# Kernel tuning notes

Measured on AMD Instinct MI355X. Metric: run time of the kernel, lower is better.

## Reference

```python
import jax, jax.numpy as jnp
import numpy as np

XYZ_MIN = -1.0
XYZ_MAX = 1.0
MULTIRES = 4  # viewdirs positional-embedding frequencies


def trilerp(grid, pts):
    """Trilinear interpolation, align_corners=True, border clamp.
    grid: [C, X, Y, Z]; pts: [N, 3] in world coords. Returns [N, C]."""
    res = np.array(grid.shape[1:])  # (X, Y, Z)
    resf = jnp.asarray(res, dtype=pts.dtype)
    u = (pts - XYZ_MIN) / (XYZ_MAX - XYZ_MIN) * (resf - 1.0)  # [N,3] voxel coords
    u = jnp.clip(u, 0.0, resf - 1.0)
    i0 = jnp.clip(jnp.floor(u).astype(jnp.int32), 0, jnp.asarray(res - 2, dtype=jnp.int32))
    f = u - i0.astype(pts.dtype)  # [N,3] fractional offsets
    out = 0.0
    for dx in (0, 1):
        wx = f[:, 0] if dx else 1.0 - f[:, 0]
        for dy in (0, 1):
            wy = f[:, 1] if dy else 1.0 - f[:, 1]
            for dz in (0, 1):
                wz = f[:, 2] if dz else 1.0 - f[:, 2]
                g = grid[:, i0[:, 0] + dx, i0[:, 1] + dy, i0[:, 2] + dz]  # [C,N]
                out = out + (wx * wy * wz) * g
    return out.T  # [N,C]


def embed_viewdirs(v):
    """NeRF positional embedding: [v, sin(2^k v), cos(2^k v)] -> [N, 3+3*2*MULTIRES]."""
    freqs = 2.0 ** jnp.arange(MULTIRES, dtype=v.dtype)  # [F]
    ang = v[:, None, :] * freqs[None, :, None]  # [N,F,3]
    n = v.shape[0]
    return jnp.concatenate([v, jnp.sin(ang).reshape(n, -1), jnp.cos(ang).reshape(n, -1)], axis=-1)


def setup_inputs() -> dict:
    key = jax.random.key(0)
    ks = jax.random.split(key, 8)
    n = 2097152
    pts = jax.random.uniform(ks[0], (n, 3), jnp.float32, minval=XYZ_MIN, maxval=XYZ_MAX)
    vd = jax.random.normal(ks[1], (n, 3), jnp.float32)
    viewdirs = vd / jnp.linalg.norm(vd, axis=-1, keepdims=True)
    density_grid = jax.random.normal(ks[2], (1, 160, 160, 160), jnp.float32)
    color_grid = jax.random.normal(ks[3], (12, 160, 160, 160), jnp.float32)
    in_dim = 9 + 3 + 3 * 2 * MULTIRES  # k0_view (12-3) + viewdirs embed (27) = 36
    w0 = jax.random.normal(ks[4], (in_dim, 128), jnp.float32) * (1.0 / np.sqrt(in_dim))
    w1 = jax.random.normal(ks[5], (128, 128), jnp.float32) * (1.0 / np.sqrt(128))
    w2 = jax.random.normal(ks[6], (128, 3), jnp.float32) * (1.0 / np.sqrt(128))
    return {
        "pts": pts, "viewdirs": viewdirs,
        "density_grid": density_grid, "color_grid": color_grid,
        "w0": w0, "b0": jnp.zeros((128,), jnp.float32),
        "w1": w1, "b1": jnp.zeros((128,), jnp.float32),
        "w2": w2, "b2": jnp.zeros((3,), jnp.float32),
    }


def reference(pts, viewdirs, density_grid, color_grid, w0, b0, w1, b1, w2, b2):
    # density branch (use_densitynet=False -> raw interpolated density, channels=1)
    pts_density = trilerp(density_grid, pts)  # [N,1]
    # color branch with color_emission: k0 = [diffuse(3), view-dep(9)]
    k0 = trilerp(color_grid, pts)  # [N,12]
    k0_diffuse, k0_view = k0[:, :3], k0[:, 3:]
    feat = jnp.concatenate([k0_view, embed_viewdirs(viewdirs)], axis=-1)  # [N,36]
    h = jax.nn.relu(feat @ w0 + b0)
    h = jax.nn.relu(h @ w1 + b1)
    k0_logit = h @ w2 + b2  # [N,3]
    pts_color = jax.nn.sigmoid(k0_logit + k0_diffuse)
    return jnp.concatenate([pts_color, pts_density], axis=-1)  # [N,4]
```

## Files before the change

### kernel.cpp

```cpp
#include <hip/hip_runtime.h>
#include <hip/hip_bf16.h>
#include <math.h>

#define RES   160
#define RES2  (160*160)
#define RES3  (160*160*160)
#define TG_ELEMS ((size_t)RES3 * 16)
#define TG_BYTES (TG_ELEMS * 2)

#define CG16_BYTES ((size_t)RES3 * 16)

#define BLOB_BYTES  47104
#define BLOB_SHORTS 22528
#define BLOB_FLOATS 512
#define A1_OFF      12288
#define B1P_OFF     45056
#define W2P_OFF     45568

typedef __attribute__((ext_vector_type(8)))  short s16x8;
typedef __attribute__((ext_vector_type(2)))  float f32x2;
typedef __attribute__((ext_vector_type(4)))  float f32x4;
typedef __attribute__((ext_vector_type(16))) float f32x16;
typedef __attribute__((ext_vector_type(4)))  int   i32x4;

__device__ __forceinline__ unsigned short f2bf(float x) {
    union { float f; unsigned u; } v; v.f = x;
    unsigned r = v.u + 0x7FFFu + ((v.u >> 16) & 1u);
    return (unsigned short)(r >> 16);
}
__device__ __forceinline__ unsigned cvtpk(float lo, float hi) {
    unsigned r;
    asm("v_cvt_pk_bf16_f32 %0, %1, %2" : "=v"(r) : "v"(lo), "v"(hi));
    return r;
}
__device__ __forceinline__ float bf_lo(unsigned u) {
    union { unsigned u; float f; } v; v.u = u << 16; return v.f;
}
__device__ __forceinline__ float bf_hi(unsigned u) {
    union { unsigned u; float f; } v; v.u = u & 0xFFFF0000u; return v.f;
}
__device__ __forceinline__ unsigned cvtpk_relu(float a, float b) {
    return cvtpk(fmaxf(a, 0.0f), fmaxf(b, 0.0f));
}
__device__ __forceinline__ void plswap(unsigned &a, unsigned &b) {
    asm("v_permlane32_swap_b32 %0, %1" : "+v"(a), "+v"(b));
}
__device__ __forceinline__ float sum_halves(float x) {
    unsigned a = __float_as_uint(x), b = a;
    plswap(a, b);
    return __uint_as_float(a) + __uint_as_float(b);
}
__device__ __forceinline__ f32x2 pkfma(f32x2 a, f32x2 b, f32x2 c) {
    f32x2 r;
    asm("v_pk_fma_f32 %0, %1, %2, %3" : "=v"(r) : "v"(a), "v"(b), "v"(c));
    return r;
}
__device__ __forceinline__ f32x2 pkmul(f32x2 a, f32x2 b) {
    f32x2 r;
    asm("v_pk_mul_f32 %0, %1, %2" : "=v"(r) : "v"(a), "v"(b));
    return r;
}

__device__ __forceinline__ unsigned enc8_manual(float x) {
    unsigned u = __float_as_uint(x);
    unsigned s = (u >> 24) & 0x80u;
    unsigned mag = u & 0x7FFFFFFFu;
    if (mag < 0x3C800000u) return s;
    if (mag >= 0x43E00000u) return s | 0x7Eu;
    unsigned r = mag + 0x7FFFFu + ((mag >> 20) & 1u);
    return s | ((r >> 20) - 960u);
}
__device__ __forceinline__ float dec8_manual(unsigned b) {
    unsigned s = (b & 0x80u) << 24;
    unsigned em = b & 0x7Fu;
    if (em == 0) return __uint_as_float(s);
    if (em < 8) {
        float v = (float)em * 0.001953125f;
        return (b & 0x80u) ? -v : v;
    }
    return __uint_as_float(s | ((em + 960u) << 20));
}
template<bool HI>
__device__ __forceinline__ unsigned pk_enc8(float a, float b, unsigned old) {
#if __has_builtin(__builtin_amdgcn_cvt_pk_fp8_f32)
    return (unsigned)__builtin_amdgcn_cvt_pk_fp8_f32(a, b, (int)old, HI);
#else
    unsigned w = enc8_manual(a) | (enc8_manual(b) << 8);
    return HI ? ((old & 0xFFFFu) | (w << 16)) : ((old & 0xFFFF0000u) | w);
#endif
}
template<bool HI>
__device__ __forceinline__ f32x2 pk_dec8(unsigned w) {
#if __has_builtin(__builtin_amdgcn_cvt_pk_f32_fp8)
    return __builtin_amdgcn_cvt_pk_f32_fp8((int)w, HI);
#else
    unsigned h = HI ? (w >> 16) : (w & 0xFFFFu);
    return f32x2{ dec8_manual(h & 0xFFu), dec8_manual((h >> 8) & 0xFFu) };
#endif
}

__device__ __forceinline__ float blob_short_val(int i, const float* __restrict__ w0,
                                                const float* __restrict__ b0,
                                                const float* __restrict__ w1) {
    if (i < 6144) {
        int e = i & 7, s = i >> 3;
        int lo = s & 31, r = s >> 5;
        int hi = r & 1, t = r >> 1;
        int wm = t / 3, ks = t - wm * 3;
        int k = ks * 16 + hi * 8 + e, n = wm * 32 + lo;
        return k < 36 ? w0[k * 128 + n] : (k == 36 ? b0[n] : 0.0f);
    } else {
        int i2 = i - 6144;
        int e = i2 & 7, s = i2 >> 3;
        int lo = s & 31, r = s >> 5;
        int hi = r & 1, t = r >> 1;
        int wm = t >> 3, ks = t & 7;
        int k = ks * 16 + hi * 8 + e, n = wm * 32 + lo;
        return w1[k * 128 + n];
    }
}
__device__ __forceinline__ float blob_float_val(int j, const float* __restrict__ b1,
                                                const float* __restrict__ w2) {
    if (j < 128) {
        int c = j & 3, r = j >> 2, hi = r & 1, t = r >> 1;
        int g = t & 3, wm = t >> 2;
        return b1[wm * 32 + 8 * g + 4 * hi + c];
    } else {
        int j2 = j - 128;
        int c  = j2 & 3;
        int t  = j2 >> 2;
        int cc = t % 3;
        int u  = t / 3;
        int hi = u & 1, v = u >> 1;
        int g  = v & 3, wm = v >> 2;
        return w2[(wm * 32 + 8 * g + 4 * hi + c) * 3 + cc];
    }
}

__global__ __launch_bounds__(256) void make_tg(
    const float* __restrict__ dgrid, const float* __restrict__ cgrid,
    short* __restrict__ tg)
{
    const int v = blockIdx.x * 256 + threadIdx.x;
    float vals[13];
    #pragma unroll
    for (int c = 0; c < 12; ++c) vals[c] = cgrid[(size_t)c * RES3 + v];
    vals[12] = dgrid[v];

    i32x4 r0 = { (int)cvtpk(vals[0], vals[1]),  (int)cvtpk(vals[2],  vals[3]),
                 (int)cvtpk(vals[4], vals[5]),  (int)cvtpk(vals[6],  vals[7]) };
    i32x4 r1 = { (int)cvtpk(vals[8], vals[9]),  (int)cvtpk(vals[10], vals[11]),
                 (int)cvtpk(vals[12], 0.0f),    0 };
    *(i32x4*)&tg[(size_t)v * 16 + 0] = r0;
    *(i32x4*)&tg[(size_t)v * 16 + 8] = r1;
}

__global__ __launch_bounds__(256) void make_cg16(
    const float* __restrict__ dgrid, const float* __restrict__ cgrid,
    char* __restrict__ cg16)
{
    const int v = blockIdx.x * 256 + threadIdx.x;
    float vals[13];
    #pragma unroll
    for (int c = 0; c < 12; ++c) vals[c] = cgrid[(size_t)c * RES3 + v];
    vals[12] = dgrid[v];

    unsigned w0 = pk_enc8<false>(vals[3], vals[4], 0u);
    w0 = pk_enc8<true>(vals[5], vals[6], w0);
    unsigned w1 = pk_enc8<false>(vals[7], vals[8], 0u);
    w1 = pk_enc8<true>(vals[9], vals[10], w1);
    unsigned w2 = pk_enc8<false>(vals[11], vals[0], 0u);
    w2 = pk_enc8<true>(vals[1], vals[2], w2);
    unsigned w3 = (unsigned)f2bf(vals[12]);

    i32x4 r = { (int)w0, (int)w1, (int)w2, (int)w3 };
    *(i32x4*)(cg16 + (size_t)v * 16) = r;
}

__global__ __launch_bounds__(256) void prepack(
    const float* __restrict__ w0, const float* __restrict__ b0,
    const float* __restrict__ w1, const float* __restrict__ b1,
    const float* __restrict__ w2, char* __restrict__ blob)
{
    int t = blockIdx.x * 256 + threadIdx.x;
    if (t < BLOB_SHORTS) {
        ((short*)blob)[t] = (short)f2bf(blob_short_val(t, w0, b0, w1));
    } else if (t < BLOB_SHORTS + BLOB_FLOATS) {
        int j = t - BLOB_SHORTS;
        ((float*)(blob + B1P_OFF))[j] = blob_float_val(j, b1, w2);
    }
}

template<int MODE, bool PRE>
__global__ __launch_bounds__(512, 4) void dvgo_fused(
    const float* __restrict__ pts, const float* __restrict__ vdirs,
    const float* __restrict__ dgrid, const float* __restrict__ cgrid,
    const short* __restrict__ tg, const char* __restrict__ cg16,
    const char* __restrict__ blob,
    const float* __restrict__ w0, const float* __restrict__ b0,
    const float* __restrict__ w1, const float* __restrict__ b1,
    const float* __restrict__ w2, const float* __restrict__ b2,
    float* __restrict__ out)
{
    __shared__ __align__(16) char smem[BLOB_BYTES];
    const int tid  = threadIdx.x;
    const int lane = tid & 63;
    const int wv   = tid >> 6;
    const int lo   = lane & 31;
    const int hi   = lane >> 5;

    if (PRE) {
        const i32x4* src = (const i32x4*)blob;
        i32x4* dst = (i32x4*)smem;
        for (int i = tid; i < BLOB_BYTES / 16; i += 512) dst[i] = src[i];
    } else {
        for (int i = tid; i < BLOB_SHORTS; i += 512)
            ((short*)smem)[i] = (short)f2bf(blob_short_val(i, w0, b0, w1));
        for (int i = tid; i < BLOB_FLOATS; i += 512)
            ((float*)(smem + B1P_OFF))[i] = blob_float_val(i, b1, w2);
    }

    const int p = blockIdx.x * 512 + tid;
    float P0 = pts[p*3+0], P1 = pts[p*3+1], P2 = pts[p*3+2];
    float V0 = vdirs[p*3+0], V1 = vdirs[p*3+1], V2 = vdirs[p*3+2];

    int   ii[3];
    float ff[3];
    float Pv[3] = {P0, P1, P2};
    #pragma unroll
    for (int d = 0; d < 3; ++d) {
        float u = (Pv[d] + 1.0f) * 79.5f;
        u = fminf(fmaxf(u, 0.0f), 159.0f);
        int i0 = (int)u;
        if (i0 > 158) i0 = 158;
        ii[d] = i0;
        ff[d] = u - (float)i0;
    }
    const float fx = ff[0], fy = ff[1], fz = ff[2];
    const float wxy0 = (1.0f-fx)*(1.0f-fy);
    const float wxy1 = (1.0f-fx)*fy;
    const float wxy2 = fx*(1.0f-fy);
    const float wxy3 = fx*fy;

    float dens;
    float col[12];

    if (MODE == 2) {
        const size_t vidx = (size_t)(ii[0] * RES + ii[1]) * RES + ii[2];
        const char* q00 = cg16 + vidx * 16;
        const char* q01 = q00 + (size_t)RES * 16;
        const char* q10 = q00 + (size_t)RES2 * 16;
        const char* q11 = q10 + (size_t)RES * 16;

        f32x2 cv[7];
        #pragma unroll
        for (int pr = 0; pr < 7; ++pr) cv[pr] = f32x2{0.0f, 0.0f};
        float densacc = 0.0f;

        const char* qs[4] = { q00, q01, q10, q11 };
        const float wsx[4] = { wxy0, wxy1, wxy2, wxy3 };
        #pragma unroll
        for (int cn = 0; cn < 4; ++cn) {
            const char* q = qs[cn];
            i32x4 A = *(const i32x4*)(q);
            i32x4 B = *(const i32x4*)(q + 16);
            const f32x2 wv2 = { wsx[cn], wsx[cn] };

            f32x2 a, b, lz;
            a = pk_dec8<false>((unsigned)A[0]); b = pk_dec8<false>((unsigned)B[0]);
            lz = pkfma(f32x2{fz,fz}, f32x2{b.x-a.x, b.y-a.y}, a);
            cv[0] = pkfma(wv2, lz, cv[0]);
            a = pk_dec8<true >((unsigned)A[0]); b = pk_dec8<true >((unsigned)B[0]);
            lz = pkfma(f32x2{fz,fz}, f32x2{b.x-a.x, b.y-a.y}, a);
            cv[1] = pkfma(wv2, lz, cv[1]);
            a = pk_dec8<false>((unsigned)A[1]); b = pk_dec8<false>((unsigned)B[1]);
            lz = pkfma(f32x2{fz,fz}, f32x2{b.x-a.x, b.y-a.y}, a);
            cv[2] = pkfma(wv2, lz, cv[2]);
            a = pk_dec8<true >((unsigned)A[1]); b = pk_dec8<true >((unsigned)B[1]);
            lz = pkfma(f32x2{fz,fz}, f32x2{b.x-a.x, b.y-a.y}, a);
            cv[3] = pkfma(wv2, lz, cv[3]);
            a = pk_dec8<false>((unsigned)A[2]); b = pk_dec8<false>((unsigned)B[2]);
            lz = pkfma(f32x2{fz,fz}, f32x2{b.x-a.x, b.y-a.y}, a);
            cv[4] = pkfma(wv2, lz, cv[4]);
            a = pk_dec8<true >((unsigned)A[2]); b = pk_dec8<true >((unsigned)B[2]);
            lz = pkfma(f32x2{fz,fz}, f32x2{b.x-a.x, b.y-a.y}, a);
            cv[5] = pkfma(wv2, lz, cv[5]);
            float da = bf_lo((unsigned)A[3]), db = bf_lo((unsigned)B[3]);
            densacc = __builtin_fmaf(wsx[cn], __builtin_fmaf(fz, db - da, da), densacc);
        }
        col[3] = cv[0].x; col[4]  = cv[0].y;
        col[5] = cv[1].x; col[6]  = cv[1].y;
        col[7] = cv[2].x; col[8]  = cv[2].y;
        col[9] = cv[3].x; col[10] = cv[3].y;
        col[11] = cv[4].x; col[0] = cv[4].y;
        col[1] = cv[5].x; col[2]  = cv[5].y;
        dens = densacc;
    } else if (MODE == 1) {
        const int base16 = ((ii[0]*RES + ii[1])*RES + ii[2]) * 16;
        const short* q00 = tg + base16;
        const short* q01 = q00 + RES*16;
        const short* q10 = q00 + RES2*16;
        const short* q11 = q10 + RES*16;

        f32x2 cv[7];
        #pragma unroll
        for (int pr = 0; pr < 7; ++pr) cv[pr] = f32x2{0.0f, 0.0f};
        const f32x2 fzv   = { fz, fz };
        const f32x2 omfzv = { 1.0f - fz, 1.0f - fz };
        const short* qs[4] = { q00, q01, q10, q11 };
        const float  wsx[4] = { wxy0, wxy1, wxy2, wxy3 };
        #pragma unroll
        for (int cn = 0; cn < 4; ++cn) {
            const short* q = qs[cn];
            i32x4 u0 = *(const i32x4*)(q);
            i32x4 u1v = *(const i32x4*)(q + 8);
            i32x4 u2 = *(const i32x4*)(q + 16);
            i32x4 u3 = *(const i32x4*)(q + 24);
            unsigned av[8] = { (unsigned)u0[0], (unsigned)u0[1], (unsigned)u0[2], (unsigned)u0[3],
                               (unsigned)u1v[0], (unsigned)u1v[1], (unsigned)u1v[2], (unsigned)u1v[3] };
            unsigned bv[8] = { (unsigned)u2[0], (unsigned)u2[1], (unsigned)u2[2], (unsigned)u2[3],
                               (unsigned)u3[0], (unsigned)u3[1], (unsigned)u3[2], (unsigned)u3[3] };
            const f32x2 wv2 = { wsx[cn], wsx[cn] };
            #pragma unroll
            for (int pr = 0; pr < 7; ++pr) {
                f32x2 va = { bf_lo(av[pr]), bf_hi(av[pr]) };
                f32x2 vb = { bf_lo(bv[pr]), bf_hi(bv[pr]) };
                f32x2 lz = pkfma(fzv, vb, pkmul(omfzv, va));
                cv[pr] = pkfma(wv2, lz, cv[pr]);
            }
        }
        #pragma unroll
        for (int c = 0; c < 12; ++c) col[c] = (c & 1) ? cv[c >> 1].y : cv[c >> 1].x;
        dens = cv[6].x;
    } else {
        const int base = (ii[0]*RES + ii[1])*RES + ii[2];
        const int o0 = base, o1 = base + RES, o2 = base + RES2, o3 = base + RES2 + RES;
        auto tl = [&](const float* __restrict__ g) -> float {
            float a0 = g[o0], a1 = g[o0+1];
            float c0 = g[o1], c1 = g[o1+1];
            float d0 = g[o2], d1 = g[o2+1];
            float e0 = g[o3], e1 = g[o3+1];
            float v0 = a0 + fz*(a1-a0);
            float v1 = c0 + fz*(c1-c0);
            float v2 = d0 + fz*(d1-d0);
            float v3 = e0 + fz*(e1-e0);
            return wxy0*v0 + wxy1*v1 + wxy2*v2 + wxy3*v3;
        };
        dens = tl(dgrid);
        #pragma unroll
        for (int c = 0; c < 12; ++c) col[c] = tl(cgrid + (size_t)c * RES3);
    }

    float ft[36];
    #pragma unroll
    for (int j = 0; j < 9; ++j) ft[j] = col[3+j];
    ft[9] = V0; ft[10] = V1; ft[11] = V2;
    float Vv[3] = {V0, V1, V2};
    #pragma unroll
    for (int d = 0; d < 3; ++d) {
        float s1, c1;
        __sincosf(Vv[d], &s1, &c1);
        float s2 = 2.0f*s1*c1,  c2 = __builtin_fmaf(-2.0f*s1, s1, 1.0f);
        float s4 = 2.0f*s2*c2,  c4 = __builtin_fmaf(-2.0f*s2, s2, 1.0f);
        float s8 = 2.0f*s4*c4,  c8 = __builtin_fmaf(-2.0f*s4, s4, 1.0f);
        ft[12 + d] = s1; ft[15 + d] = s2; ft[18 + d] = s4; ft[21 + d] = s8;
        ft[24 + d] = c1; ft[27 + d] = c2; ft[30 + d] = c4; ft[33 + d] = c8;
    }
    unsigned fpk[24];
    #pragma unroll
    for (int j = 0; j < 18; ++j) fpk[j] = cvtpk(ft[2*j], ft[2*j+1]);
    fpk[18] = cvtpk(1.0f, 0.0f);
    #pragma unroll
    for (int j = 19; j < 24; ++j) fpk[j] = 0u;

    #pragma unroll
    for (int ks = 0; ks < 3; ++ks)
        #pragma unroll
        for (int d = 0; d < 4; ++d)
            plswap(fpk[ks*8 + d], fpk[ks*8 + 4 + d]);

    const float col0v = col[0], col1v = col[1], col2v = col[2];
    const float scol0 = __shfl_xor(col0v, 32, 64);
    const float scol1 = __shfl_xor(col1v, 32, 64);
    const float scol2 = __shfl_xor(col2v, 32, 64);
    const float sdens = __shfl_xor(dens,  32, 64);
    const float b2v0 = b2[0], b2v1 = b2[1], b2v2 = b2[2];

    __syncthreads();

    const char*  a0p  = smem + lane * 16;
    const char*  a1p  = smem + A1_OFF + lane * 16;
    const float* b1ph = (const float*)(smem + B1P_OFF) + hi * 4;
    const float* w2ph = (const float*)(smem + W2P_OFF) + hi * 12;

    #pragma unroll
    for (int pt = 0; pt < 2; ++pt) {
        f32x16 acc0[4];
        #pragma unroll
        for (int w = 0; w < 4; ++w)
            #pragma unroll
            for (int r = 0; r < 16; ++r) acc0[w][r] = 0.0f;

        #pragma unroll
        for (int ks = 0; ks < 3; ++ks) {
            i32x4 bi = { (int)fpk[ks*8 + 4*pt + 0], (int)fpk[ks*8 + 4*pt + 1],
                         (int)fpk[ks*8 + 4*pt + 2], (int)fpk[ks*8 + 4*pt + 3] };
            s16x8 B = __builtin_bit_cast(s16x8, bi);
            #pragma unroll
            for (int w = 0; w < 4; ++w) {
                s16x8 A = *(const s16x8*)(a0p + (w*3 + ks) * 1024);
                acc0[w] = __builtin_amdgcn_mfma_f32_32x32x16_bf16(A, B, acc0[w], 0, 0, 0);
            }
        }

        unsigned u1[4][8];
        #pragma unroll
        for (int w = 0; w < 4; ++w)
            #pragma unroll
            for (int g = 0; g < 4; ++g) {
                u1[w][2*g+0] = cvtpk_relu(acc0[w][4*g+0], acc0[w][4*g+1]);
                u1[w][2*g+1] = cvtpk_relu(acc0[w][4*g+2], acc0[w][4*g+3]);
            }

        f32x16 acc1[4];
        #pragma unroll
        for (int w = 0; w < 4; ++w)
            #pragma unroll
            for (int g = 0; g < 4; ++g) {
                f32x4 bv = *(const f32x4*)(b1ph + (w*4 + g) * 8);
                acc1[w][4*g+0] = bv[0]; acc1[w][4*g+1] = bv[1];
                acc1[w][4*g+2] = bv[2]; acc1[w][4*g+3] = bv[3];
            }
        #pragma unroll
        for (int ks = 0; ks < 8; ++ks) {
            const int w = ks >> 1, q = 4 * (ks & 1);
            plswap(u1[w][q+0], u1[w][q+2]);
            plswap(u1[w][q+1], u1[w][q+3]);
            i32x4 bi = { (int)u1[w][q+0], (int)u1[w][q+1],
                         (int)u1[w][q+2], (int)u1[w][q+3] };
            s16x8 B = __builtin_bit_cast(s16x8, bi);
            #pragma unroll
            for (int wm = 0; wm < 4; ++wm) {
                s16x8 A = *(const s16x8*)(a1p + (wm*8 + ks) * 1024);
                acc1[wm] = __builtin_amdgcn_mfma_f32_32x32x16_bf16(A, B, acc1[wm], 0, 0, 0);
            }
        }

        f32x2 pa0 = {0.0f, 0.0f}, pa1 = {0.0f, 0.0f}, pa2 = {0.0f, 0.0f};
        #pragma unroll
        for (int w = 0; w < 4; ++w)
            #pragma unroll
            for (int g = 0; g < 4; ++g) {
                const float* wrow = w2ph + (w*4 + g) * 24;
                f32x4 q0 = *(const f32x4*)(wrow + 0);
                f32x4 q1 = *(const f32x4*)(wrow + 4);
                f32x4 q2 = *(const f32x4*)(wrow + 8);
                f32x2 v01 = { fmaxf(acc1[w][4*g+0], 0.0f), fmaxf(acc1[w][4*g+1], 0.0f) };
                f32x2 v23 = { fmaxf(acc1[w][4*g+2], 0.0f), fmaxf(acc1[w][4*g+3], 0.0f) };
                pa0 = pkfma(v01, f32x2{q0[0], q0[1]}, pa0);
                pa0 = pkfma(v23, f32x2{q0[2], q0[3]}, pa0);
                pa1 = pkfma(v01, f32x2{q1[0], q1[1]}, pa1);
                pa1 = pkfma(v23, f32x2{q1[2], q1[3]}, pa1);
                pa2 = pkfma(v01, f32x2{q2[0], q2[1]}, pa2);
                pa2 = pkfma(v23, f32x2{q2[2], q2[3]}, pa2);
            }
        float p0 = sum_halves(pa0.x + pa0.y);
        float p1 = sum_halves(pa1.x + pa1.y);
        float p2 = sum_halves(pa2.x + pa2.y);

        const float d0 = pt ? scol0 : col0v;
        const float d1 = pt ? scol1 : col1v;
        const float d2 = pt ? scol2 : col2v;
        const float dn = pt ? sdens : dens;
        if (hi == 0) {
            float x0 = p0 + b2v0 + d0;
            float x1 = p1 + b2v1 + d1;
            float x2 = p2 + b2v2 + d2;
            f32x4 o = { 1.0f / (1.0f + __expf(-x0)),
                        1.0f / (1.0f + __expf(-x1)),
                        1.0f / (1.0f + __expf(-x2)),
                        dn };
            const int gp = blockIdx.x * 512 + wv * 64 + pt * 32 + lo;
            *(f32x4*)(out + (size_t)gp * 4) = o;
        }
    }
}

extern "C" void kernel_launch(void* const* d_in, const int* in_sizes, int n_in,
                              void* d_out, int out_size, void* d_ws, size_t ws_size,
                              hipStream_t stream) {
    const float* pts = (const float*)d_in[0];
    const float* vd  = (const float*)d_in[1];
    const float* dg  = (const float*)d_in[2];
    const float* cg  = (const float*)d_in[3];
    const float* w0  = (const float*)d_in[4];
    const float* b0  = (const float*)d_in[5];
    const float* w1  = (const float*)d_in[6];
    const float* b1  = (const float*)d_in[7];
    const float* w2  = (const float*)d_in[8];
    const float* b2  = (const float*)d_in[9];
    float* out = (float*)d_out;

    const int n = in_sizes[0] / 3;
    const int blocks = n / 512;

    if (ws_size >= CG16_BYTES + BLOB_BYTES) {
        char* cg16 = (char*)d_ws;
        char* blob = (char*)d_ws + CG16_BYTES;
        make_cg16<<<RES3/256, 256, 0, stream>>>(dg, cg, cg16);
        prepack<<<(BLOB_SHORTS + BLOB_FLOATS + 255)/256, 256, 0, stream>>>(
            w0, b0, w1, b1, w2, blob);
        dvgo_fused<2, true><<<blocks, 512, 0, stream>>>(
            pts, vd, dg, cg, nullptr, cg16, blob, w0, b0, w1, b1, w2, b2, out);
    } else if (ws_size >= TG_BYTES + BLOB_BYTES) {
        short* tg = (short*)d_ws;
        char* blob = (char*)d_ws + TG_BYTES;
        make_tg<<<RES3/256, 256, 0, stream>>>(dg, cg, tg);
        prepack<<<(BLOB_SHORTS + BLOB_FLOATS + 255)/256, 256, 0, stream>>>(
            w0, b0, w1, b1, w2, blob);
        dvgo_fused<1, true><<<blocks, 512, 0, stream>>>(
            pts, vd, dg, cg, tg, nullptr, blob, w0, b0, w1, b1, w2, b2, out);
    } else if (ws_size >= TG_BYTES) {
        short* tg = (short*)d_ws;
        make_tg<<<RES3/256, 256, 0, stream>>>(dg, cg, tg);
        dvgo_fused<1, false><<<blocks, 512, 0, stream>>>(
            pts, vd, dg, cg, tg, nullptr, nullptr, w0, b0, w1, b1, w2, b2, out);
    } else {
        dvgo_fused<0, false><<<blocks, 512, 0, stream>>>(
            pts, vd, dg, cg, nullptr, nullptr, nullptr, w0, b0, w1, b1, w2, b2, out);
    }
}
```

Before: 246.2 us.

## Pack 2x2 yz-neighborhood per voxel into 64-byte records for trilinear gathers

Adds a preprocessing kernel that, for each voxel, stores the four y/z neighbours of all 12 colour channels in fp8 and the density in bf16, giving one 64-byte record per voxel. The fused kernel then needs only two contiguous 64-byte reads (x and x+1) per sample instead of four scattered 32-byte pairs, and interpolates with nested lerps. The cost is a four times larger intermediate grid (about 262 MB) to build each call and more preprocessing traffic, and the new path runs only when the workspace is large enough.

```diff
diff --git a/kernel.cpp b/kernel.cpp
--- a/kernel.cpp
+++ b/kernel.cpp
@@ -9,6 +9,8 @@
 #define TG_BYTES (TG_ELEMS * 2)
 
 #define CG16_BYTES ((size_t)RES3 * 16)
+
+#define QG64_BYTES ((size_t)RES3 * 64)
 
 #define BLOB_BYTES  47104
 #define BLOB_SHORTS 22528
@@ -97,6 +99,14 @@
     unsigned h = HI ? (w >> 16) : (w & 0xFFFFu);
     return f32x2{ dec8_manual(h & 0xFFu), dec8_manual((h >> 8) & 0xFFu) };
 #endif
+}
+
+__device__ __forceinline__ float quad_lerp(unsigned w, float fy, float fz) {
+    f32x2 lo = pk_dec8<false>(w);
+    f32x2 hi = pk_dec8<true >(w);
+    float vy0 = __builtin_fmaf(fz, lo.y - lo.x, lo.x);
+    float vy1 = __builtin_fmaf(fz, hi.y - hi.x, hi.x);
+    return __builtin_fmaf(fy, vy1 - vy0, vy0);
 }
 
 __device__ __forceinline__ float blob_short_val(int i, const float* __restrict__ w0,
@@ -177,6 +187,47 @@
     *(i32x4*)(cg16 + (size_t)v * 16) = r;
 }
 
+__global__ __launch_bounds__(256) void make_quad(
+    const float* __restrict__ dgrid, const float* __restrict__ cgrid,
+    char* __restrict__ qg)
+{
+    const int v = blockIdx.x * 256 + threadIdx.x;
+    const int z = v % RES;
+    const int xy = v / RES;
+    const int y = xy % RES;
+    const int dz = (z < RES-1) ? 1 : 0;
+    const int dy = (y < RES-1) ? RES : 0;
+    const int o00 = v, o01 = v + dz, o10 = v + dy, o11 = v + dy + dz;
+
+    unsigned words[16];
+    #pragma unroll
+    for (int c = 0; c < 13; ++c) {
+        float c00, c01, c10, c11;
+        if (c < 9) {
+            const float* g = cgrid + (size_t)(3 + c) * RES3;
+            c00 = g[o00]; c01 = g[o01]; c10 = g[o10]; c11 = g[o11];
+        } else if (c < 12) {
+            const float* g = cgrid + (size_t)(c - 9) * RES3;
+            c00 = g[o00]; c01 = g[o01]; c10 = g[o10]; c11 = g[o11];
+        } else {
+            c00 = c01 = c10 = c11 = 0.0f;
+        }
+        unsigned w = pk_enc8<false>(c00, c01, 0u);
+        words[c] = pk_enc8<true>(c10, c11, w);
+    }
+    words[13] = cvtpk(dgrid[o00], dgrid[o01]);
+    words[14] = cvtpk(dgrid[o10], dgrid[o11]);
+    words[15] = 0u;
+
+    char* dst = qg + (size_t)v * 64;
+    #pragma unroll
+    for (int s = 0; s < 4; ++s) {
+        i32x4 r = { (int)words[4*s+0], (int)words[4*s+1],
+                    (int)words[4*s+2], (int)words[4*s+3] };
+        *(i32x4*)(dst + s * 16) = r;
+    }
+}
+
 __global__ __launch_bounds__(256) void prepack(
     const float* __restrict__ w0, const float* __restrict__ b0,
     const float* __restrict__ w1, const float* __restrict__ b1,
@@ -195,7 +246,7 @@
 __global__ __launch_bounds__(512, 4) void dvgo_fused(
     const float* __restrict__ pts, const float* __restrict__ vdirs,
     const float* __restrict__ dgrid, const float* __restrict__ cgrid,
-    const short* __restrict__ tg, const char* __restrict__ cg16,
+    const short* __restrict__ tg, const char* __restrict__ gq,
     const char* __restrict__ blob,
     const float* __restrict__ w0, const float* __restrict__ b0,
     const float* __restrict__ w1, const float* __restrict__ b1,
@@ -237,17 +288,46 @@
         ff[d] = u - (float)i0;
     }
     const float fx = ff[0], fy = ff[1], fz = ff[2];
-    const float wxy0 = (1.0f-fx)*(1.0f-fy);
-    const float wxy1 = (1.0f-fx)*fy;
-    const float wxy2 = fx*(1.0f-fy);
-    const float wxy3 = fx*fy;
 
     float dens;
     float col[12];
 
-    if (MODE == 2) {
+    if (MODE == 3) {
         const size_t vidx = (size_t)(ii[0] * RES + ii[1]) * RES + ii[2];
-        const char* q00 = cg16 + vidx * 16;
+        const char* qa = gq + vidx * 64;
+        const char* qb = qa + (size_t)RES2 * 64;
+        i32x4 A[4], B[4];
+        #pragma unroll
+        for (int s = 0; s < 4; ++s) A[s] = *(const i32x4*)(qa + s * 16);
+        #pragma unroll
+        for (int s = 0; s < 4; ++s) B[s] = *(const i32x4*)(qb + s * 16);
+
+        #pragma unroll
+        for (int c = 0; c < 12; ++c) {
+            float va = quad_lerp((unsigned)A[c >> 2][c & 3], fy, fz);
+            float vb = quad_lerp((unsigned)B[c >> 2][c & 3], fy, fz);
+            float val = __builtin_fmaf(fx, vb - va, va);
+            if (c < 9) col[3 + c] = val;
+            else       col[c - 9] = val;
+        }
+        {
+            unsigned a13 = (unsigned)A[3][1], a14 = (unsigned)A[3][2];
+            unsigned b13 = (unsigned)B[3][1], b14 = (unsigned)B[3][2];
+            float ay0 = __builtin_fmaf(fz, bf_hi(a13) - bf_lo(a13), bf_lo(a13));
+            float ay1 = __builtin_fmaf(fz, bf_hi(a14) - bf_lo(a14), bf_lo(a14));
+            float va  = __builtin_fmaf(fy, ay1 - ay0, ay0);
+            float by0 = __builtin_fmaf(fz, bf_hi(b13) - bf_lo(b13), bf_lo(b13));
+            float by1 = __builtin_fmaf(fz, bf_hi(b14) - bf_lo(b14), bf_lo(b14));
+            float vb  = __builtin_fmaf(fy, by1 - by0, by0);
+            dens = __builtin_fmaf(fx, vb - va, va);
+        }
+    } else if (MODE == 2) {
+        const float wxy0 = (1.0f-fx)*(1.0f-fy);
+        const float wxy1 = (1.0f-fx)*fy;
+        const float wxy2 = fx*(1.0f-fy);
+        const float wxy3 = fx*fy;
+        const size_t vidx = (size_t)(ii[0] * RES + ii[1]) * RES + ii[2];
+        const char* q00 = gq + vidx * 16;
         const char* q01 = q00 + (size_t)RES * 16;
         const char* q10 = q00 + (size_t)RES2 * 16;
         const char* q11 = q10 + (size_t)RES * 16;
@@ -265,7 +345,6 @@
             i32x4 A = *(const i32x4*)(q);
             i32x4 B = *(const i32x4*)(q + 16);
             const f32x2 wv2 = { wsx[cn], wsx[cn] };
-
             f32x2 a, b, lz;
             a = pk_dec8<false>((unsigned)A[0]); b = pk_dec8<false>((unsigned)B[0]);
             lz = pkfma(f32x2{fz,fz}, f32x2{b.x-a.x, b.y-a.y}, a);
@@ -296,6 +375,10 @@
         col[1] = cv[5].x; col[2]  = cv[5].y;
         dens = densacc;
     } else if (MODE == 1) {
+        const float wxy0 = (1.0f-fx)*(1.0f-fy);
+        const float wxy1 = (1.0f-fx)*fy;
+        const float wxy2 = fx*(1.0f-fy);
+        const float wxy3 = fx*fy;
         const int base16 = ((ii[0]*RES + ii[1])*RES + ii[2]) * 16;
         const short* q00 = tg + base16;
         const short* q01 = q00 + RES*16;
@@ -333,6 +416,10 @@
         for (int c = 0; c < 12; ++c) col[c] = (c & 1) ? cv[c >> 1].y : cv[c >> 1].x;
         dens = cv[6].x;
     } else {
+        const float wxy0 = (1.0f-fx)*(1.0f-fy);
+        const float wxy1 = (1.0f-fx)*fy;
+        const float wxy2 = fx*(1.0f-fy);
+        const float wxy3 = fx*fy;
         const int base = (ii[0]*RES + ii[1])*RES + ii[2];
         const int o0 = base, o1 = base + RES, o2 = base + RES2, o3 = base + RES2 + RES;
         auto tl = [&](const float* __restrict__ g) -> float {
@@ -504,7 +591,15 @@
     const int n = in_sizes[0] / 3;
     const int blocks = n / 512;
 
-    if (ws_size >= CG16_BYTES + BLOB_BYTES) {
+    if (ws_size >= QG64_BYTES + BLOB_BYTES) {
+        char* qg = (char*)d_ws;
+        char* blob = (char*)d_ws + QG64_BYTES;
+        make_quad<<<RES3/256, 256, 0, stream>>>(dg, cg, qg);
+        prepack<<<(BLOB_SHORTS + BLOB_FLOATS + 255)/256, 256, 0, stream>>>(
+            w0, b0, w1, b1, w2, blob);
+        dvgo_fused<3, true><<<blocks, 512, 0, stream>>>(
+            pts, vd, dg, cg, nullptr, qg, blob, w0, b0, w1, b1, w2, b2, out);
+    } else if (ws_size >= CG16_BYTES + BLOB_BYTES) {
         char* cg16 = (char*)d_ws;
         char* blob = (char*)d_ws + CG16_BYTES;
         make_cg16<<<RES3/256, 256, 0, stream>>>(dg, cg, cg16);
```

Measured after the change: 277.9 us. 12.9% more time.
